# Kernel tuning notes

Measured on AMD Instinct MI355X. Metric: run time of the kernel, lower is better.

The kernel has to match this reference:

```python
import jax, jax.numpy as jnp
import numpy as np

N_BR, BATCH, HID, ARR = 8, 128, 512, 256


def setup_inputs() -> dict:
    key = jax.random.key(0)
    ks = jax.random.split(key, 9)
    s = 0.05  # small init scale to keep gates unsaturated
    return {
        "x": jax.random.normal(ks[0], (N_BR, BATCH, ARR), jnp.float32),
        "c": jax.random.normal(ks[1], (BATCH, ARR, 1), jnp.float32),
        "Wih": jax.random.normal(ks[2], (N_BR, 4 * HID, 1), jnp.float32) * s,
        "Whh": jax.random.normal(ks[3], (N_BR, 4 * HID, HID), jnp.float32) * s,
        "b_ih": jax.random.normal(ks[4], (N_BR, 4 * HID), jnp.float32) * s,
        "b_hh": jax.random.normal(ks[5], (N_BR, 4 * HID), jnp.float32) * s,
        "hn0": jnp.zeros((N_BR, BATCH, HID), jnp.float32),
        "Wl": jax.random.normal(ks[6], (N_BR, ARR), jnp.float32) * s,
        "bl": jax.random.normal(ks[7], (N_BR,), jnp.float32) * s,
    }


def reference(x, c, Wih, Whh, b_ih, b_hh, hn0, Wl, bl):
    # x: (n_br, B, T) -- the per-branch multiplier p
    # c: (B, T, 1)    -- shared scalar input sequence for every branch's LSTM
    bias = (b_ih + b_hh)[:, None, :]            # (n, 1, 4H)
    xs = jnp.swapaxes(c, 0, 1)                  # (T, B, 1)
    c0 = jnp.zeros_like(hn0)                    # torch `zeros` global as cell state

    def step(carry, x_t):
        h, cc = carry                           # each (n, B, H)
        gates = (jnp.einsum('nbh,ngh->nbg', h, Whh)
                 + jnp.einsum('bi,ngi->nbg', x_t, Wih)
                 + bias)                        # (n, B, 4H), gate order i,f,g,o
        i, f, g, o = jnp.split(gates, 4, axis=-1)
        cc = jax.nn.sigmoid(f) * cc + jax.nn.sigmoid(i) * jnp.tanh(g)
        h = jax.nn.sigmoid(o) * jnp.tanh(cc)
        return (h, cc), h[:, :, -1]             # o[:, :, -1]: last hidden feature

    _, ys = jax.lax.scan(step, (hn0, c0), xs)   # ys: (T, n, B)
    # stack(map(...)).sum(0): sum_n (o[:,:,-1] * p) -> (B, T)
    r = jnp.einsum('tnb,nbt->bt', ys, x)
    return r @ Wl.T + bl                        # Linear(arr_size -> n_br)
```

## Files before the change

### kernel.cpp

```cpp
#include <hip/hip_runtime.h>


#define NBR   8
#define BATCH 128
#define HIDN  512
#define TLEN  256

typedef __attribute__((ext_vector_type(8))) short bf16x8;
typedef __attribute__((ext_vector_type(4))) float f32x4;

__device__ __forceinline__ unsigned short bf16_rne(float f) {
  unsigned int u = __float_as_uint(f);
  u += 0x7FFFu + ((u >> 16) & 1u);
  return (unsigned short)(u >> 16);
}

__device__ __forceinline__ float sigm(float x) {
  return __builtin_amdgcn_rcpf(1.0f + __expf(-x));
}
__device__ __forceinline__ float tanh_(float x) {
  float ax = fabsf(x);
  float e  = __expf(-2.0f * ax);
  float t  = (1.0f - e) * __builtin_amdgcn_rcpf(1.0f + e);
  return copysignf(t, x);
}

#define HLOADX(d, p, OFF, SC) \
  asm volatile("global_load_dwordx4 %0, %1, off offset:" OFF " " SC \
               : "=v"(d) : "v"(p))
#define DLOADX(d, p, SC) \
  asm volatile("global_load_dword %0, %1, off " SC : "=v"(d) : "v"(p))
#define DLOADF(d, p, SC) \
  asm volatile("global_load_dword %0, %1, off " SC : "=v"(d) : "v"(p))
#define QSTOREX(p, v, SC) \
  asm volatile("global_store_dwordx2 %0, %1, off " SC \
               :: "v"(p), "v"(v) : "memory")
#define QSTOREXO(p, v, OFF, SC) \
  asm volatile("global_store_dwordx2 %0, %1, off offset:" OFF " " SC \
               :: "v"(p), "v"(v) : "memory")
#define DSTOREX(p, v, SC) \
  asm volatile("global_store_dword %0, %1, off " SC \
               :: "v"(p), "v"(v) : "memory")
#define WAITV(N) asm volatile("s_waitcnt vmcnt(" #N ")" ::: "memory")
#define INVL1() asm volatile("buffer_inv sc0" ::: "memory")
#define SCHEDB() __builtin_amdgcn_sched_barrier(0)
#define AUMAX_NR(p, v, SC) \
  asm volatile("global_atomic_umax %0, %1, off " SC :: "v"(p), "v"(v) : "memory")
#define AUMAX_RET(d, p, v, SC) \
  asm volatile("global_atomic_umax %0, %1, %2, off " SC \
               : "=v"(d) : "v"(p), "v"(v) : "memory")

#define LOAD_H(SC) do {                         \
    HLOADX(hvv[0][0], pc, "0",   SC);           \
    HLOADX(hvv[0][1], pc, "64",  SC);           \
    HLOADX(hvv[0][2], pc, "128", SC);           \
    HLOADX(hvv[0][3], pc, "192", SC);           \
    HLOADX(hvv[1][0], pc, "256", SC);           \
    HLOADX(hvv[1][1], pc, "320", SC);           \
    HLOADX(hvv[1][2], pc, "384", SC);           \
    HLOADX(hvv[1][3], pc, "448", SC);           \
    HLOADX(hvv[2][0], pc, "512", SC);           \
    HLOADX(hvv[2][1], pc, "576", SC);           \
    HLOADX(hvv[2][2], pc, "640", SC);           \
    HLOADX(hvv[2][3], pc, "704", SC);           \
    HLOADX(hvv[3][0], pc, "768", SC);           \
    HLOADX(hvv[3][1], pc, "832", SC);           \
    HLOADX(hvv[3][2], pc, "896", SC);           \
    HLOADX(hvv[3][3], pc, "960", SC);           \
  } while (0)

#define MFMA_CHUNK(C) do {                                                    \
    _Pragma("unroll")                                                         \
    for (int k4 = 0; k4 < 4; ++k4) {                                          \
      bf16x8 hfrag = __builtin_bit_cast(bf16x8, hvv[C][k4]);                  \
      _Pragma("unroll")                                                       \
      for (int tt = 0; tt < 8; ++tt) {                                        \
        bf16x8 wf = __builtin_bit_cast(bf16x8,                                \
            Wlds[tt * 1024 + (4 * (C) + k4) * 64 + wb]);                      \
        acc[tt] = __builtin_amdgcn_mfma_f32_16x16x32_bf16(                    \
            wf, hfrag, acc[tt], 0, 0, 0);                                     \
      }                                                                       \
    }                                                                         \
  } while (0)

#define STEP_LOOP(SC, FM)                                                     \
  for (int t = 0; t < TLEN; ++t) {                                            \
    f32x4 acc[8];                                                             \
    _Pragma("unroll")                                                         \
    for (int tt = 0; tt < 8; ++tt) acc[tt] = (f32x4){0.f, 0.f, 0.f, 0.f};     \
    const char* pc = curB + hoff;                                             \
    uint4 hvv[4][4];                                                          \
    float cv;                                                                 \
    DLOADF(cv, c_ptr + t, "");                                                \
    LOAD_H(SC);                                                               \
    WAITV(12); SCHEDB(); MFMA_CHUNK(0);                                       \
    WAITV(8);  SCHEDB(); MFMA_CHUNK(1);                                       \
    WAITV(4);  SCHEDB(); MFMA_CHUNK(2);                                       \
    WAITV(0);  SCHEDB(); MFMA_CHUNK(3);                                       \
    _Pragma("unroll")                                                         \
    for (int u = 0; u < 2; ++u) {                                             \
      unsigned lo = 0, hi = 0;                                                \
      _Pragma("unroll")                                                       \
      for (int r = 0; r < 4; ++r) {                                           \
        float2 pI = Bp[ 0 + u * 16 + q4 + r];                                 \
        float2 pF = Bp[32 + u * 16 + q4 + r];                                 \
        float2 pG = Bp[64 + u * 16 + q4 + r];                                 \
        float2 pO = Bp[96 + u * 16 + q4 + r];                                 \
        float gi = acc[0 + u][r] + pI.x * cv + pI.y;                          \
        float gf = acc[2 + u][r] + pF.x * cv + pF.y;                          \
        float gg = acc[4 + u][r] + pG.x * cv + pG.y;                          \
        float go = acc[6 + u][r] + pO.x * cv + pO.y;                          \
        float ncc = sigm(gf) * cc[u][r] + sigm(gi) * tanh_(gg);               \
        cc[u][r] = ncc;                                                       \
        float hval = sigm(go) * tanh_(ncc);                                   \
        unsigned hb = bf16_rne(hval);                                         \
        if (r == 0) lo = hb;                                                  \
        if (r == 1) lo |= hb << 16;                                           \
        if (r == 2) hi = hb;                                                  \
        if (r == 3) hi |= hb << 16;                                           \
        if (u == 1 && r == 3 && jt == 15 && q == 3)                           \
          ys[t * (NBR * BATCH) + n * BATCH + bb] = hval;                      \
      }                                                                       \
      unsigned long long pack =                                               \
          (unsigned long long)lo | ((unsigned long long)hi << 32);            \
      QSTOREX(nxtB + (u ? soff1 : soff0), pack, SC);                          \
    }                                                                         \
    if (t == TLEN - 1) break;                                                 \
    WAITV(0);                                         \
    const unsigned tgt = (unsigned)(t + 1);                                   \
    if (FM) {                                                                 \
      if (lane == 0) { AUMAX_NR(myflag, tgt, "");                             \
                       AUMAX_NR(myflag, tgt, "sc1"); }                        \
      int spins = 0;                                                          \
      for (;;) {                                                              \
        unsigned fv = 0xFFFFFFFFu;                                            \
        if (lane < 16) {                                                      \
          if (spins < 256) { AUMAX_RET(fv, ppoll, 0u, "sc0"); }               \
          else             { AUMAX_RET(fv, ppoll, 0u, "sc0 sc1"); }           \
        }                                                                     \
        WAITV(0); SCHEDB();                                                   \
        if (__all((int)(fv >= tgt))) break;                                   \
        ++spins; __builtin_amdgcn_s_sleep(1);                                 \
      }                                                                       \
      INVL1(); WAITV(0);             \
    } else {                                                                  \
      if (lane == 0) DSTOREX(myflag, tgt, "sc0 sc1");                         \
      for (;;) {                                                              \
        unsigned f0v;                                                         \
        DLOADX(f0v, pf0, "sc0 sc1");                                          \
        WAITV(0); SCHEDB();                                                   \
        if (__all((int)(f0v >= tgt))) break;                                  \
        __builtin_amdgcn_s_sleep(1);                                          \
      }                                                                       \
    }                                                                         \
    char* tsw = curB; curB = nxtB; nxtB = tsw;                                \
  }

__global__ __launch_bounds__(256, 1) void lstm_main(
    const float* __restrict__ c_in,
    const float* __restrict__ Wih,
    const float* __restrict__ Whh,
    const float* __restrict__ b_ih,
    const float* __restrict__ b_hh,
    char* __restrict__ hImp,
    char* __restrict__ hPure,
    float* __restrict__ ys,
    unsigned int* __restrict__ iflags,
    unsigned int* __restrict__ pflags,
    unsigned int* __restrict__ vx,
    unsigned int* __restrict__ vdict,
    unsigned int* __restrict__ ibar)
{
  __shared__ uint4 Wlds[8192];
  __shared__ float2 Bp[128];
  __shared__ unsigned sflag;

  const int tid  = threadIdx.x;
  const int lane = tid & 63;
  const int w    = tid >> 6;
  const int ln15 = lane & 15;
  const int q    = lane >> 4;
  const int q4   = q * 4;
  const int n    = blockIdx.x & 7;
  const int m    = blockIdx.x >> 3;
  const int jt   = m & 15;
  const int bt   = m >> 4;
  const int j0   = jt << 5;
  const int wb   = q * 16 + ln15;

  unsigned xcc_raw;
  asm volatile("s_getreg_b32 %0, hwreg(HW_REG_XCC_ID)" : "=s"(xcc_raw));
  const unsigned xcc = xcc_raw & 0xFu;
  if (tid == 0) { sflag = 0; DSTOREX(&vx[blockIdx.x], 0xA5000000u | xcc, "sc0 sc1"); }

  for (int idx = tid; idx < 8192; idx += 256) {
    int ln   = idx & 15;
    int q_   = (idx >> 4) & 3;
    int ks_  = (idx >> 6) & 15;
    int tile = idx >> 10;
    int g_   = tile >> 1;
    int uu   = tile & 1;
    const float* src = Whh +
        (size_t)(n * 2048 + g_ * 512 + j0 + uu * 16 + ln) * 512 + ks_ * 32 + q_ * 8;
    float4 f0 = *(const float4*)(src);
    float4 f1 = *(const float4*)(src + 4);
    uint4 v;
    v.x = (unsigned)bf16_rne(f0.x) | ((unsigned)bf16_rne(f0.y) << 16);
    v.y = (unsigned)bf16_rne(f0.z) | ((unsigned)bf16_rne(f0.w) << 16);
    v.z = (unsigned)bf16_rne(f1.x) | ((unsigned)bf16_rne(f1.y) << 16);
    v.w = (unsigned)bf16_rne(f1.z) | ((unsigned)bf16_rne(f1.w) << 16);
    Wlds[idx] = v;
  }
  if (tid < 128) {
    int g = n * 2048 + (tid >> 5) * 512 + j0 + (tid & 31);
    Bp[tid] = make_float2(Wih[g], b_ih[g] + b_hh[g]);
  }

  if (m == 0 && w == 0) {
    const unsigned ref = 0xA5000000u | xcc;
    unsigned v0 = 0, v1 = 0, v2 = 0, v3 = 0;
    int ok = 0;
    for (int it = 0; it < 16384; ++it) {
      DLOADX(v0, &vx[lane],       "sc0 sc1");
      DLOADX(v1, &vx[lane + 64],  "sc0 sc1");
      DLOADX(v2, &vx[lane + 128], "sc0 sc1");
      DLOADX(v3, &vx[lane + 192], "sc0 sc1");
      WAITV(0);
      if (__all((int)(((v0 & 0xFF000000u) == 0xA5000000u) &&
                      ((v1 & 0xFF000000u) == 0xA5000000u) &&
                      ((v2 & 0xFF000000u) == 0xA5000000u) &&
                      ((v3 & 0xFF000000u) == 0xA5000000u)))) { ok = 1; break; }
      __builtin_amdgcn_s_sleep(1);
    }
    unsigned verdict = 0;
    if (ok) {
      const bool mine = ((lane & 7) == n);
      int uni = __all((int)(!mine || (v0 == ref && v1 == ref && v2 == ref && v3 == ref)));
      int oth = __all((int)( mine || (v0 != ref && v1 != ref && v2 != ref && v3 != ref)));
      verdict = (uni && oth && (xcc < 8u)) ? 1u : 0u;
    }
    if (lane == 0)
      DSTOREX(&vdict[n], 0xB5000000u | (verdict << 8) | xcc, "sc0 sc1");
  }

  unsigned vd;
  for (;;) {
    DLOADX(vd, &vdict[n], "sc0 sc1");
    WAITV(0);
    if ((vd & 0xFF000000u) == 0xB5000000u) break;
    __builtin_amdgcn_s_sleep(2);
  }
  const int pure   = (int)((vd >> 8) & 1u);
  const unsigned x = vd & 0xFu;

  const int bb = bt * 64 + w * 16 + ln15;
  const size_t hoff  = (size_t)bb * 1024 + (size_t)q * 16;
  const size_t soff0 = (size_t)bb * 1024 + (size_t)(j0 + q4) * 2;
  const size_t soff1 = soff0 + 32;
  const float* c_ptr = c_in + (size_t)bb * 256;

  float cc[2][4];
#pragma unroll
  for (int u = 0; u < 2; ++u)
#pragma unroll
    for (int r = 0; r < 4; ++r) cc[u][r] = 0.0f;

  char *curB, *nxtB;
  unsigned int *flagB, *myflag;
  const unsigned int *ppoll, *pf0;
  if (pure) {
    curB = hPure + (size_t)x * 262144; nxtB = curB + 131072;
    flagB  = pflags + x * 2048;
    myflag = flagB + ((bt * 4 + w) * 16 + jt) * 16;
    ppoll  = flagB + ((bt * 4 + w) * 16 + (lane & 15)) * 16;
    pf0    = flagB;
  } else {
    curB = hImp + (size_t)n * 131072; nxtB = curB + (size_t)NBR * 131072;
    flagB  = iflags + n * 128;
    myflag = flagB + m * 4 + w;
    ppoll  = flagB;
    pf0    = flagB + bt * 64 + lane;
  }

  __syncthreads();

  if (pure) {
    char* rp = hPure + (size_t)x * 262144 + (size_t)m * 8192;
    for (int i = tid; i < 1024; i += 256)
      QSTOREXO(rp + (size_t)i * 8, 0ull, "0", "sc0");
    if (lane == 0) {
      DSTOREX(myflag, 0u, "sc0");
      WAITV(0);
      DSTOREX(myflag, 0u, "sc0 sc1");
    }
    WAITV(0);
    __syncthreads();
    if (tid == 0) DSTOREX(&ibar[x * 32 + m], 1u, "sc0 sc1");
    for (;;) {
      unsigned iv;
      DLOADX(iv, &ibar[x * 32 + (lane & 31)], "sc0 sc1");
      WAITV(0);
      if (__all((int)(iv >= 1u))) break;
      __builtin_amdgcn_s_sleep(2);
    }
    INVL1(); WAITV(0);
    STEP_LOOP("", 1)
  } else {
    STEP_LOOP("sc0 sc1", 0)
  }
}

__global__ __launch_bounds__(256) void finalize_k(
    const float* __restrict__ ys, const float* __restrict__ x,
    const float* __restrict__ Wl, const float* __restrict__ bl,
    float* __restrict__ out)
{
  int b = blockIdx.x;
  int tid = threadIdx.x;
  __shared__ float r[256];
  float acc = 0.f;
#pragma unroll
  for (int n = 0; n < NBR; ++n)
    acc += ys[tid * (NBR * BATCH) + n * BATCH + b] * x[(n * BATCH + b) * 256 + tid];
  r[tid] = acc;
  __syncthreads();
  int wv = tid >> 6, ln = tid & 63;
#pragma unroll
  for (int jj = 0; jj < 2; ++jj) {
    int j = wv * 2 + jj;
    float p = 0.f;
#pragma unroll
    for (int t2 = ln; t2 < 256; t2 += 64) p += r[t2] * Wl[j * 256 + t2];
#pragma unroll
    for (int s = 32; s > 0; s >>= 1) p += __shfl_down(p, s, 64);
    if (ln == 0) out[b * NBR + j] = p + bl[j];
  }
}

extern "C" void kernel_launch(void* const* d_in, const int* in_sizes, int n_in,
                              void* d_out, int out_size, void* d_ws, size_t ws_size,
                              hipStream_t stream) {
  const float* x    = (const float*)d_in[0];
  const float* c    = (const float*)d_in[1];
  const float* Wih  = (const float*)d_in[2];
  const float* Whh  = (const float*)d_in[3];
  const float* b_ih = (const float*)d_in[4];
  const float* b_hh = (const float*)d_in[5];
  const float* Wl   = (const float*)d_in[7];
  const float* bl   = (const float*)d_in[8];
  float* out = (float*)d_out;

  char* ws = (char*)d_ws;
  char*  hImp  = ws;
  char*  hPure = ws + (2u << 20);
  float* ys    = (float*)(ws + (4u << 20));
  unsigned int* ctrl   = (unsigned int*)(ws + (5u << 20));
  unsigned int* iflags = ctrl;
  unsigned int* pflags = ctrl + 1024;
  unsigned int* vx     = ctrl + 17408;
  unsigned int* vdict  = ctrl + 17664;
  unsigned int* ibar   = ctrl + 17672;

  (void)hipMemsetAsync(hImp, 0, 1u << 20, stream);
  (void)hipMemsetAsync(ctrl, 0, 17928u * sizeof(unsigned int), stream);

  lstm_main<<<256, 256, 0, stream>>>(c, Wih, Whh, b_ih, b_hh, hImp, hPure, ys,
                                     iflags, pflags, vx, vdict, ibar);
  finalize_k<<<BATCH, 256, 0, stream>>>(ys, x, Wl, bl, out);
}
```

Measured before the change: 1.292 ms.

## Merge batch-half blocks into 512-thread blocks sharing one LDS weight copy

Halves the grid from 256 to 128 blocks of 512 threads, so each block covers both batch halves for its hidden-column tile and the Whh tile is converted and staged into LDS once per block instead of twice. The per-step flag layout and polling change to match: the impure path polls per-warp, per-tile flags instead of a single block flag, and the init barrier waits on 16 blocks. The aim is fewer participants in the cross-block step synchronisation and less duplicated weight loading. The trade-off is that only 128 CUs are used and each CU runs twice as many waves.

```diff
diff --git a/kernel.cpp b/kernel.cpp
--- a/kernel.cpp
+++ b/kernel.cpp
@@ -147,7 +147,7 @@
       if (lane == 0) DSTOREX(myflag, tgt, "sc0 sc1");                         \
       for (;;) {                                                              \
         unsigned f0v;                                                         \
-        DLOADX(f0v, pf0, "sc0 sc1");                                          \
+        DLOADX(f0v, ipoll, "sc0 sc1");                                        \
         WAITV(0); SCHEDB();                                                   \
         if (__all((int)(f0v >= tgt))) break;                                  \
         __builtin_amdgcn_s_sleep(1);                                          \
@@ -156,7 +156,7 @@
     char* tsw = curB; curB = nxtB; nxtB = tsw;                                \
   }
 
-__global__ __launch_bounds__(256, 1) void lstm_main(
+__global__ __launch_bounds__(512, 1) void lstm_main(
     const float* __restrict__ c_in,
     const float* __restrict__ Wih,
     const float* __restrict__ Whh,
@@ -173,7 +173,6 @@
 {
   __shared__ uint4 Wlds[8192];
   __shared__ float2 Bp[128];
-  __shared__ unsigned sflag;
 
   const int tid  = threadIdx.x;
   const int lane = tid & 63;
@@ -182,18 +181,18 @@
   const int q    = lane >> 4;
   const int q4   = q * 4;
   const int n    = blockIdx.x & 7;
-  const int m    = blockIdx.x >> 3;
-  const int jt   = m & 15;
-  const int bt   = m >> 4;
+  const int jt   = blockIdx.x >> 3;
   const int j0   = jt << 5;
+  const int team = w >> 2;
+  const int wsub = w & 3;
   const int wb   = q * 16 + ln15;
 
   unsigned xcc_raw;
   asm volatile("s_getreg_b32 %0, hwreg(HW_REG_XCC_ID)" : "=s"(xcc_raw));
   const unsigned xcc = xcc_raw & 0xFu;
-  if (tid == 0) { sflag = 0; DSTOREX(&vx[blockIdx.x], 0xA5000000u | xcc, "sc0 sc1"); }
-
-  for (int idx = tid; idx < 8192; idx += 256) {
+  if (tid == 0) DSTOREX(&vx[blockIdx.x], 0xA5000000u | xcc, "sc0 sc1");
+
+  for (int idx = tid; idx < 8192; idx += 512) {
     int ln   = idx & 15;
     int q_   = (idx >> 4) & 3;
     int ks_  = (idx >> 6) & 15;
@@ -216,27 +215,23 @@
     Bp[tid] = make_float2(Wih[g], b_ih[g] + b_hh[g]);
   }
 
-  if (m == 0 && w == 0) {
+  if (jt == 0 && w == 0) {
     const unsigned ref = 0xA5000000u | xcc;
-    unsigned v0 = 0, v1 = 0, v2 = 0, v3 = 0;
+    unsigned v0 = 0, v1 = 0;
     int ok = 0;
     for (int it = 0; it < 16384; ++it) {
-      DLOADX(v0, &vx[lane],       "sc0 sc1");
-      DLOADX(v1, &vx[lane + 64],  "sc0 sc1");
-      DLOADX(v2, &vx[lane + 128], "sc0 sc1");
-      DLOADX(v3, &vx[lane + 192], "sc0 sc1");
+      DLOADX(v0, &vx[lane],      "sc0 sc1");
+      DLOADX(v1, &vx[lane + 64], "sc0 sc1");
       WAITV(0);
       if (__all((int)(((v0 & 0xFF000000u) == 0xA5000000u) &&
-                      ((v1 & 0xFF000000u) == 0xA5000000u) &&
-                      ((v2 & 0xFF000000u) == 0xA5000000u) &&
-                      ((v3 & 0xFF000000u) == 0xA5000000u)))) { ok = 1; break; }
+                      ((v1 & 0xFF000000u) == 0xA5000000u)))) { ok = 1; break; }
       __builtin_amdgcn_s_sleep(1);
     }
     unsigned verdict = 0;
     if (ok) {
       const bool mine = ((lane & 7) == n);
-      int uni = __all((int)(!mine || (v0 == ref && v1 == ref && v2 == ref && v3 == ref)));
-      int oth = __all((int)( mine || (v0 != ref && v1 != ref && v2 != ref && v3 != ref)));
+      int uni = __all((int)(!mine || (v0 == ref && v1 == ref)));
+      int oth = __all((int)( mine || (v0 != ref && v1 != ref)));
       verdict = (uni && oth && (xcc < 8u)) ? 1u : 0u;
     }
     if (lane == 0)
@@ -253,7 +248,7 @@
   const int pure   = (int)((vd >> 8) & 1u);
   const unsigned x = vd & 0xFu;
 
-  const int bb = bt * 64 + w * 16 + ln15;
+  const int bb = team * 64 + wsub * 16 + ln15;
   const size_t hoff  = (size_t)bb * 1024 + (size_t)q * 16;
   const size_t soff0 = (size_t)bb * 1024 + (size_t)(j0 + q4) * 2;
   const size_t soff1 = soff0 + 32;
@@ -266,27 +261,27 @@
     for (int r = 0; r < 4; ++r) cc[u][r] = 0.0f;
 
   char *curB, *nxtB;
-  unsigned int *flagB, *myflag;
-  const unsigned int *ppoll, *pf0;
+  unsigned int *myflag;
+  const unsigned int *ppoll, *ipoll;
   if (pure) {
     curB = hPure + (size_t)x * 262144; nxtB = curB + 131072;
-    flagB  = pflags + x * 2048;
-    myflag = flagB + ((bt * 4 + w) * 16 + jt) * 16;
-    ppoll  = flagB + ((bt * 4 + w) * 16 + (lane & 15)) * 16;
-    pf0    = flagB;
+    unsigned int* flagB = pflags + x * 2048;
+    myflag = flagB + (w * 16 + jt) * 16;
+    ppoll  = flagB + (w * 16 + (lane & 15)) * 16;
+    ipoll  = flagB;
   } else {
     curB = hImp + (size_t)n * 131072; nxtB = curB + (size_t)NBR * 131072;
-    flagB  = iflags + n * 128;
-    myflag = flagB + m * 4 + w;
+    unsigned int* flagB = iflags + n * 128;
+    myflag = flagB + w * 16 + jt;
+    ipoll  = flagB + w * 16 + (lane & 15);
     ppoll  = flagB;
-    pf0    = flagB + bt * 64 + lane;
   }
 
   __syncthreads();
 
   if (pure) {
-    char* rp = hPure + (size_t)x * 262144 + (size_t)m * 8192;
-    for (int i = tid; i < 1024; i += 256)
+    char* rp = hPure + (size_t)x * 262144 + (size_t)jt * 16384;
+    for (int i = tid; i < 2048; i += 512)
       QSTOREXO(rp + (size_t)i * 8, 0ull, "0", "sc0");
     if (lane == 0) {
       DSTOREX(myflag, 0u, "sc0");
@@ -295,10 +290,10 @@
     }
     WAITV(0);
     __syncthreads();
-    if (tid == 0) DSTOREX(&ibar[x * 32 + m], 1u, "sc0 sc1");
+    if (tid == 0) DSTOREX(&ibar[x * 32 + jt], 1u, "sc0 sc1");
     for (;;) {
       unsigned iv;
-      DLOADX(iv, &ibar[x * 32 + (lane & 31)], "sc0 sc1");
+      DLOADX(iv, &ibar[x * 32 + (lane & 15)], "sc0 sc1");
       WAITV(0);
       if (__all((int)(iv >= 1u))) break;
       __builtin_amdgcn_s_sleep(2);
@@ -364,7 +359,7 @@
   (void)hipMemsetAsync(hImp, 0, 1u << 20, stream);
   (void)hipMemsetAsync(ctrl, 0, 17928u * sizeof(unsigned int), stream);
 
-  lstm_main<<<256, 256, 0, stream>>>(c, Wih, Whh, b_ih, b_hh, hImp, hPure, ys,
+  lstm_main<<<128, 512, 0, stream>>>(c, Wih, Whh, b_ih, b_hh, hImp, hPure, ys,
                                      iflags, pflags, vx, vdict, ibar);
   finalize_k<<<BATCH, 256, 0, stream>>>(ys, x, Wl, bl, out);
 }
```

Result: slower. 1.547 ms (+19.7%).
